# Kernel optimization log

Measured on AMD Instinct MI355X. Metric: run time of the kernel, lower is better.

## Reference

```python
import jax, jax.numpy as jnp
import numpy as np

HID = 64        # HIDDEN_DIM
SLOTS = 6       # MEMORY_SLOTS
V = 64          # VOCAB_SIZE
NH = 2          # attention heads
THRESH = 0.5    # STAGE1_THRESH
EPS = 1e-5      # LayerNorm eps (torch default)


def setup_inputs() -> dict:
    key = jax.random.key(0)
    ks = jax.random.split(key, 16)
    B, L = 64, 1024
    def n(k, shape, s=0.05):
        return jax.random.normal(k, shape, jnp.float32) * s
    return {
        'seq':    jax.random.randint(ks[0], (B, L), 0, V),
        'query':  jax.random.randint(ks[1], (B,), 0, V),
        'target': jax.random.randint(ks[2], (B,), 0, V),
        # TinyEncoder params
        'embed':   n(ks[3], (V, HID)),
        'wqkv':    n(ks[4], (3 * HID, HID)), 'bqkv': jnp.zeros(3 * HID, jnp.float32),
        'wo_attn': n(ks[5], (HID, HID)),     'bo_attn': jnp.zeros(HID, jnp.float32),
        'w_ff1':   n(ks[6], (2 * HID, HID)), 'b_ff1': jnp.zeros(2 * HID, jnp.float32),
        'w_ff2':   n(ks[7], (HID, 2 * HID)), 'b_ff2': jnp.zeros(HID, jnp.float32),
        'g1': jnp.ones(HID, jnp.float32), 'be1': jnp.zeros(HID, jnp.float32),
        'g2': jnp.ones(HID, jnp.float32), 'be2': jnp.zeros(HID, jnp.float32),
        # gates
        'w_s1': n(ks[8], (1, HID)), 'b_s1': jnp.zeros(1, jnp.float32),
        'w_s2': n(ks[9], (1, HID)), 'b_s2': jnp.zeros(1, jnp.float32),
        # MemoryReader
        'w_qr': n(ks[10], (HID, HID)), 'b_qr': jnp.zeros(HID, jnp.float32),
        'w_or': n(ks[11], (V, HID)),   'b_or': jnp.zeros(V, jnp.float32),
        # query embedding
        'q_embed': n(ks[12], (V, HID)),
    }


def _layernorm(x, g, b):
    m = x.mean(-1, keepdims=True)
    v = ((x - m) ** 2).mean(-1, keepdims=True)
    return (x - m) * jax.lax.rsqrt(v + EPS) * g + b


def _mha(h, wqkv, bqkv, wo, bo):
    B, L, H = h.shape
    d = H // NH
    qkv = h @ wqkv.T + bqkv                      # [B,L,3H]
    q, k, v = jnp.split(qkv, 3, axis=-1)
    q = q.reshape(B, L, NH, d)
    k = k.reshape(B, L, NH, d)
    v = v.reshape(B, L, NH, d)
    scores = jnp.einsum('bqhd,bkhd->bhqk', q, k) / jnp.sqrt(jnp.float32(d))
    w = jax.nn.softmax(scores, axis=-1)          # [B,NH,L,L]
    o = jnp.einsum('bhqk,bkhd->bqhd', w, v).reshape(B, L, H)
    return o @ wo.T + bo


def reference(seq, query, target, embed, wqkv, bqkv, wo_attn, bo_attn,
              w_ff1, b_ff1, w_ff2, b_ff2, g1, be1, g2, be2,
              w_s1, b_s1, w_s2, b_s2, w_qr, b_qr, w_or, b_or, q_embed):
    # --- TinyEncoder ---
    h = embed[seq]                                           # [B,L,H]
    a = _mha(h, wqkv, bqkv, wo_attn, bo_attn)
    h = _layernorm(h + a, g1, be1)
    ff = jax.nn.relu(h @ w_ff1.T + b_ff1) @ w_ff2.T + b_ff2
    hidden = _layernorm(h + ff, g2, be2)                     # [B,L,H]

    # --- two-stage selection (vectorized; dead s1-branch elided) ---
    s1 = jax.nn.sigmoid(jnp.squeeze(hidden @ w_s1.T + b_s1, -1))   # [B,L]
    keep = (s1 > THRESH).astype(hidden.dtype)
    s2 = jax.nn.sigmoid(jnp.squeeze(hidden @ w_s2.T + b_s2, -1))
    s2f = s2 * keep
    _, topk = jax.lax.top_k(s2f, SLOTS)                            # [B,SLOTS]

    # --- gather memory slots ---
    mem = jnp.take_along_axis(hidden, topk[:, :, None], axis=1)    # [B,SLOTS,H]

    # --- MemoryReader ---
    q_h = q_embed[query]                                           # [B,H]
    q = q_h @ w_qr.T + b_qr                                        # [B,H]
    scores = (q[:, None, :] * mem).sum(-1) / jnp.sqrt(jnp.float32(HID))  # [B,SLOTS]
    w = jax.nn.softmax(scores, axis=-1)
    ctx = (w[:, :, None] * mem).sum(1)                             # [B,H]
    logits = ctx @ w_or.T + b_or                                   # [B,V]

    # --- cross entropy (mean) ---
    logp = jax.nn.log_softmax(logits, axis=-1)
    loss = -jnp.take_along_axis(logp, target[:, None], axis=1).mean()
    return loss
```

## Files before the change

kernel.cpp:

```cpp
#include <hip/hip_runtime.h>

#define DEV __device__ __forceinline__

DEV float wsum(float v){
  #pragma unroll
  for (int o = 32; o; o >>= 1) v += __shfl_xor(v, o, 64);
  return v;
}
DEV float wmax(float v){
  #pragma unroll
  for (int o = 32; o; o >>= 1) v = fmaxf(v, __shfl_xor(v, o, 64));
  return v;
}

__global__ __launch_bounds__(256) void k_prep(
    const int* __restrict__ seq, const float* __restrict__ embed,
    const float* __restrict__ wqkv, const float* __restrict__ bqkv,
    float* __restrict__ qkv_tab, float* __restrict__ cnt_f){
  const int b = blockIdx.x, tid = threadIdx.x;
  __shared__ float emb[64];
  __shared__ int hh[64];
  if (tid < 64){ emb[tid] = embed[b*64 + tid]; hh[tid] = 0; }
  __syncthreads();
  for (int i = tid; i < 1024; i += 256) atomicAdd(&hh[seq[b*1024 + i]], 1);
  if (tid < 192){
    const float4* w4 = (const float4*)(wqkv + tid*64);
    float acc = bqkv[tid];
    #pragma unroll
    for (int k = 0; k < 16; ++k){
      float4 w = w4[k];
      acc += w.x*emb[4*k] + w.y*emb[4*k+1] + w.z*emb[4*k+2] + w.w*emb[4*k+3];
    }
    qkv_tab[b*192 + tid] = acc;
  }
  __syncthreads();
  if (tid < 64) cnt_f[b*64 + tid] = (float)hh[tid];
}

__global__ __launch_bounds__(256) void k_enc(
    const float* __restrict__ qkv_tab, const float* __restrict__ cnt_f,
    const float* __restrict__ embed,
    const float* __restrict__ wo_attn, const float* __restrict__ bo_attn,
    const float* __restrict__ w_ff1, const float* __restrict__ b_ff1,
    const float* __restrict__ w_ff2, const float* __restrict__ b_ff2,
    const float* __restrict__ g1, const float* __restrict__ be1,
    const float* __restrict__ g2, const float* __restrict__ be2,
    const float* __restrict__ w_s1, const float* __restrict__ b_s1,
    const float* __restrict__ w_s2, const float* __restrict__ b_s2,
    float* __restrict__ hidden_tab, float* __restrict__ s2f_tab){
  const int b = blockIdx.x >> 2, quarter = blockIdx.x & 3;
  const int tid = threadIdx.x, wave = tid >> 6, lane = tid & 63;

  __shared__ float k_lds[64*65];
  __shared__ float v_lds[64*65];
  __shared__ float wo_lds[64*65];
  __shared__ float ff1_lds[128*65];
  __shared__ float ff2_lds[64*129];
  __shared__ float cnt_lds[64];
  __shared__ float xbuf[4][64];
  __shared__ float ybuf[4][128];

  for (int i = tid; i < 4096; i += 256){
    int r = i >> 6, c = i & 63;
    k_lds[r*65 + c]  = qkv_tab[r*192 + 64 + c];
    v_lds[r*65 + c]  = qkv_tab[r*192 + 128 + c];
    wo_lds[r*65 + c] = wo_attn[i];
  }
  for (int i = tid; i < 8192; i += 256){
    ff1_lds[(i >> 6)*65 + (i & 63)]   = w_ff1[i];
    ff2_lds[(i >> 7)*129 + (i & 127)] = w_ff2[i];
  }
  if (tid < 64) cnt_lds[tid] = cnt_f[b*64 + tid];
  __syncthreads();

  const float g1v = g1[lane],  be1v = be1[lane];
  const float g2v = g2[lane],  be2v = be2[lane];
  const float bov = bo_attn[lane], bf2v = b_ff2[lane];
  const float bf1a = b_ff1[lane], bf1b = b_ff1[64 + lane];
  const float ws1v = w_s1[lane], ws2v = w_s2[lane];
  const float bs1 = b_s1[0], bs2 = b_s2[0];
  const float cme = cnt_lds[lane];
  const bool  pres = cme > 0.f;
  const float sc = 0.17677669529663687f;

  #pragma unroll 1
  for (int it = 0; it < 4; ++it){
    const int tok = quarter*16 + wave*4 + it;
    const float qreg = qkv_tab[tok*192 + lane];
    float s0 = 0.f, s1v = 0.f;
    #pragma unroll
    for (int d = 0; d < 32; ++d){
      float q0 = __shfl(qreg, d, 64);
      float q1 = __shfl(qreg, 32 + d, 64);
      s0  += q0 * k_lds[lane*65 + d];
      s1v += q1 * k_lds[lane*65 + 32 + d];
    }
    s0 *= sc; s1v *= sc;
    float m0 = wmax(pres ? s0  : -1e30f);
    float m1 = wmax(pres ? s1v : -1e30f);
    float p0 = pres ? cme * __expf(s0  - m0) : 0.f;
    float p1 = pres ? cme * __expf(s1v - m1) : 0.f;
    float d0 = wsum(p0), d1 = wsum(p1);
    float o = 0.f;
    #pragma unroll
    for (int t = 0; t < 64; ++t){
      float a0 = __shfl(p0, t, 64);
      float a1 = __shfl(p1, t, 64);
      o += (lane < 32 ? a0 : a1) * v_lds[t*65 + lane];
    }
    o /= (lane < 32 ? d0 : d1);
    float a = bov;
    #pragma unroll
    for (int k = 0; k < 64; ++k) a += wo_lds[lane*65 + k] * __shfl(o, k, 64);
    float x = embed[tok*64 + lane] + a;
    float mu = wsum(x) * 0.015625f;
    float xm = x - mu;
    float var = wsum(xm*xm) * 0.015625f;
    float xn = xm * rsqrtf(var + 1e-5f) * g1v + be1v;
    xbuf[wave][lane] = xn;
    __builtin_amdgcn_wave_barrier();
    float y0 = bf1a, y1 = bf1b;
    #pragma unroll
    for (int k = 0; k < 64; ++k){
      float xk = xbuf[wave][k];
      y0 += ff1_lds[lane*65 + k] * xk;
      y1 += ff1_lds[(lane + 64)*65 + k] * xk;
    }
    y0 = fmaxf(y0, 0.f); y1 = fmaxf(y1, 0.f);
    ybuf[wave][lane] = y0; ybuf[wave][64 + lane] = y1;
    __builtin_amdgcn_wave_barrier();
    float z = bf2v;
    #pragma unroll
    for (int j = 0; j < 128; ++j) z += ff2_lds[lane*129 + j] * ybuf[wave][j];
    float r = xn + z;
    float mu2 = wsum(r) * 0.015625f;
    float rm = r - mu2;
    float var2 = wsum(rm*rm) * 0.015625f;
    float hid = rm * rsqrtf(var2 + 1e-5f) * g2v + be2v;
    float t1 = wsum(hid * ws1v) + bs1;
    float t2 = wsum(hid * ws2v) + bs2;
    float sg1 = 1.f / (1.f + __expf(-t1));
    float sg2 = 1.f / (1.f + __expf(-t2));
    float s2f = (sg1 > 0.5f) ? sg2 : 0.f;

    hidden_tab[(b*64 + tok)*64 + lane] = hid;
    if (lane == 0) s2f_tab[b*64 + tok] = s2f;
  }
}

__global__ __launch_bounds__(64) void k_sel(
    const int* __restrict__ seq, const int* __restrict__ query,
    const int* __restrict__ target,
    const float* __restrict__ hidden_tab, const float* __restrict__ s2f_tab,
    const float* __restrict__ w_qr, const float* __restrict__ b_qr,
    const float* __restrict__ w_or, const float* __restrict__ b_or,
    const float* __restrict__ q_embed, float* __restrict__ partial){
  const int b = blockIdx.x, lane = threadIdx.x;
  __shared__ float s2_lds[64];
  s2_lds[lane] = s2f_tab[b*64 + lane];
  __builtin_amdgcn_wave_barrier();

  float vals[16];
  #pragma unroll
  for (int j = 0; j < 16; ++j){
    int tk = seq[b*1024 + j*64 + lane];
    vals[j] = s2_lds[tk];
  }
  int sel[6];
  #pragma unroll
  for (int r = 0; r < 6; ++r){
    float bv = -1.f; int bi = 1 << 30;
    #pragma unroll
    for (int j = 0; j < 16; ++j){
      float v = vals[j]; int i = (j << 6) | lane;
      if (v > bv || (v == bv && i < bi)){ bv = v; bi = i; }
    }
    #pragma unroll
    for (int o = 32; o; o >>= 1){
      float ov = __shfl_xor(bv, o, 64);
      int   oi = __shfl_xor(bi, o, 64);
      if (ov > bv || (ov == bv && oi < bi)){ bv = ov; bi = oi; }
    }
    sel[r] = bi;
    int jw = bi >> 6, lw = bi & 63;
    if (lane == lw){
      #pragma unroll
      for (int j = 0; j < 16; ++j) if (j == jw) vals[j] = -1.f;
    }
  }

  float mem[6];
  #pragma unroll
  for (int s = 0; s < 6; ++s){
    int tk = seq[b*1024 + sel[s]];
    mem[s] = hidden_tab[(b*64 + tk)*64 + lane];
  }
  float qe = q_embed[query[b]*64 + lane];
  float qv = b_qr[lane];
  #pragma unroll
  for (int k = 0; k < 64; ++k) qv += w_qr[lane*64 + k] * __shfl(qe, k, 64);
  float scv[6];
  #pragma unroll
  for (int s = 0; s < 6; ++s) scv[s] = wsum(qv * mem[s]) * 0.125f;
  float mx = scv[0];
  #pragma unroll
  for (int s = 1; s < 6; ++s) mx = fmaxf(mx, scv[s]);
  float e[6], se = 0.f;
  #pragma unroll
  for (int s = 0; s < 6; ++s){ e[s] = __expf(scv[s] - mx); se += e[s]; }
  float ctx = 0.f;
  #pragma unroll
  for (int s = 0; s < 6; ++s) ctx += (e[s] / se) * mem[s];
  float lg = b_or[lane];
  #pragma unroll
  for (int k = 0; k < 64; ++k) lg += w_or[lane*64 + k] * __shfl(ctx, k, 64);
  float lm = wmax(lg);
  float ss = wsum(__expf(lg - lm));
  float lt = __shfl(lg, target[b], 64);
  if (lane == 0) partial[b] = -(lt - lm - __logf(ss));
}

__global__ __launch_bounds__(64) void k_final(const float* __restrict__ partial,
                                              float* __restrict__ out){
  float v = partial[threadIdx.x];
  v = wsum(v);
  if (threadIdx.x == 0) out[0] = v * 0.015625f;
}

extern "C" void kernel_launch(void* const* d_in, const int* in_sizes, int n_in,
                              void* d_out, int out_size, void* d_ws, size_t ws_size,
                              hipStream_t stream){
  const int*   seq     = (const int*)  d_in[0];
  const int*   query   = (const int*)  d_in[1];
  const int*   target  = (const int*)  d_in[2];
  const float* embed   = (const float*)d_in[3];
  const float* wqkv    = (const float*)d_in[4];
  const float* bqkv    = (const float*)d_in[5];
  const float* wo_attn = (const float*)d_in[6];
  const float* bo_attn = (const float*)d_in[7];
  const float* w_ff1   = (const float*)d_in[8];
  const float* b_ff1   = (const float*)d_in[9];
  const float* w_ff2   = (const float*)d_in[10];
  const float* b_ff2   = (const float*)d_in[11];
  const float* g1      = (const float*)d_in[12];
  const float* be1     = (const float*)d_in[13];
  const float* g2      = (const float*)d_in[14];
  const float* be2     = (const float*)d_in[15];
  const float* w_s1    = (const float*)d_in[16];
  const float* b_s1    = (const float*)d_in[17];
  const float* w_s2    = (const float*)d_in[18];
  const float* b_s2    = (const float*)d_in[19];
  const float* w_qr    = (const float*)d_in[20];
  const float* b_qr    = (const float*)d_in[21];
  const float* w_or    = (const float*)d_in[22];
  const float* b_or    = (const float*)d_in[23];
  const float* q_embed = (const float*)d_in[24];

  float* ws = (float*)d_ws;
  float* qkv_tab    = ws;
  float* cnt_f      = ws + 12288;
  float* hidden_tab = ws + 16384;
  float* s2f_tab    = ws + 278528;
  float* partial    = ws + 282624;

  k_prep<<<64, 256, 0, stream>>>(seq, embed, wqkv, bqkv, qkv_tab, cnt_f);
  k_enc<<<256, 256, 0, stream>>>(qkv_tab, cnt_f, embed, wo_attn, bo_attn,
                                 w_ff1, b_ff1, w_ff2, b_ff2, g1, be1, g2, be2,
                                 w_s1, b_s1, w_s2, b_s2, hidden_tab, s2f_tab);
  k_sel<<<64, 64, 0, stream>>>(seq, query, target, hidden_tab, s2f_tab,
                               w_qr, b_qr, w_or, b_or, q_embed, partial);
  k_final<<<1, 64, 0, stream>>>(partial, (float*)d_out);
}
```

Baseline: 150.1 us.

## Use one wave per token, drop final kernel via atomic loss, stage weights in LDS

The encoder kernel now launches 1024 threads per block with one wave per token, replacing the four-token sequential loop per wave. Query and probability broadcasts go through LDS instead of lane shuffles, and the dot products use multiple accumulators to expose more ILP. The reduction kernel is removed: the output is zeroed in the prep kernel and each selection block adds its scaled loss atomically. The selection kernel also stages w_qr and w_or into padded LDS. The trade-off is that the larger blocks reload the weights into LDS for every 16 tokens, and the atomic sum makes the result order nondeterministic.

```diff
diff --git a/kernel.cpp b/kernel.cpp
--- a/kernel.cpp
+++ b/kernel.cpp
@@ -13,31 +13,36 @@
   return v;
 }
 
-__global__ __launch_bounds__(256) void k_prep(
+__global__ __launch_bounds__(1024) void k_prep(
     const int* __restrict__ seq, const float* __restrict__ embed,
     const float* __restrict__ wqkv, const float* __restrict__ bqkv,
-    float* __restrict__ qkv_tab, float* __restrict__ cnt_f){
+    float* __restrict__ qkv_tab, float* __restrict__ cnt_f,
+    float* __restrict__ out){
   const int b = blockIdx.x, tid = threadIdx.x;
+  if (b == 0 && tid == 0) out[0] = 0.f;
   __shared__ float emb[64];
   __shared__ int hh[64];
   if (tid < 64){ emb[tid] = embed[b*64 + tid]; hh[tid] = 0; }
   __syncthreads();
-  for (int i = tid; i < 1024; i += 256) atomicAdd(&hh[seq[b*1024 + i]], 1);
+  atomicAdd(&hh[seq[b*1024 + tid]], 1);
   if (tid < 192){
     const float4* w4 = (const float4*)(wqkv + tid*64);
-    float acc = bqkv[tid];
+    float a0 = bqkv[tid], a1 = 0.f, a2 = 0.f, a3 = 0.f;
     #pragma unroll
-    for (int k = 0; k < 16; ++k){
-      float4 w = w4[k];
-      acc += w.x*emb[4*k] + w.y*emb[4*k+1] + w.z*emb[4*k+2] + w.w*emb[4*k+3];
+    for (int k = 0; k < 16; k += 4){
+      float4 wa = w4[k],   wb = w4[k+1], wc = w4[k+2], wd = w4[k+3];
+      a0 += wa.x*emb[4*k]    + wa.y*emb[4*k+1]  + wa.z*emb[4*k+2]  + wa.w*emb[4*k+3];
+      a1 += wb.x*emb[4*k+4]  + wb.y*emb[4*k+5]  + wb.z*emb[4*k+6]  + wb.w*emb[4*k+7];
+      a2 += wc.x*emb[4*k+8]  + wc.y*emb[4*k+9]  + wc.z*emb[4*k+10] + wc.w*emb[4*k+11];
+      a3 += wd.x*emb[4*k+12] + wd.y*emb[4*k+13] + wd.z*emb[4*k+14] + wd.w*emb[4*k+15];
     }
-    qkv_tab[b*192 + tid] = acc;
+    qkv_tab[b*192 + tid] = (a0+a1)+(a2+a3);
   }
   __syncthreads();
   if (tid < 64) cnt_f[b*64 + tid] = (float)hh[tid];
 }
 
-__global__ __launch_bounds__(256) void k_enc(
+__global__ __launch_bounds__(1024, 4) void k_enc(
     const float* __restrict__ qkv_tab, const float* __restrict__ cnt_f,
     const float* __restrict__ embed,
     const float* __restrict__ wo_attn, const float* __restrict__ bo_attn,
@@ -57,16 +62,16 @@
   __shared__ float ff1_lds[128*65];
   __shared__ float ff2_lds[64*129];
   __shared__ float cnt_lds[64];
-  __shared__ float xbuf[4][64];
-  __shared__ float ybuf[4][128];
-
-  for (int i = tid; i < 4096; i += 256){
+  __shared__ float xbuf[16][64];
+  __shared__ float pbuf[16][128];
+
+  for (int i = tid; i < 4096; i += 1024){
     int r = i >> 6, c = i & 63;
     k_lds[r*65 + c]  = qkv_tab[r*192 + 64 + c];
     v_lds[r*65 + c]  = qkv_tab[r*192 + 128 + c];
     wo_lds[r*65 + c] = wo_attn[i];
   }
-  for (int i = tid; i < 8192; i += 256){
+  for (int i = tid; i < 8192; i += 1024){
     ff1_lds[(i >> 6)*65 + (i & 63)]   = w_ff1[i];
     ff2_lds[(i >> 7)*129 + (i & 127)] = w_ff2[i];
   }
@@ -82,70 +87,90 @@
   const float cme = cnt_lds[lane];
   const bool  pres = cme > 0.f;
   const float sc = 0.17677669529663687f;
-
-  #pragma unroll 1
-  for (int it = 0; it < 4; ++it){
-    const int tok = quarter*16 + wave*4 + it;
-    const float qreg = qkv_tab[tok*192 + lane];
-    float s0 = 0.f, s1v = 0.f;
-    #pragma unroll
-    for (int d = 0; d < 32; ++d){
-      float q0 = __shfl(qreg, d, 64);
-      float q1 = __shfl(qreg, 32 + d, 64);
-      s0  += q0 * k_lds[lane*65 + d];
-      s1v += q1 * k_lds[lane*65 + 32 + d];
-    }
-    s0 *= sc; s1v *= sc;
-    float m0 = wmax(pres ? s0  : -1e30f);
-    float m1 = wmax(pres ? s1v : -1e30f);
-    float p0 = pres ? cme * __expf(s0  - m0) : 0.f;
-    float p1 = pres ? cme * __expf(s1v - m1) : 0.f;
-    float d0 = wsum(p0), d1 = wsum(p1);
-    float o = 0.f;
-    #pragma unroll
-    for (int t = 0; t < 64; ++t){
-      float a0 = __shfl(p0, t, 64);
-      float a1 = __shfl(p1, t, 64);
-      o += (lane < 32 ? a0 : a1) * v_lds[t*65 + lane];
-    }
-    o /= (lane < 32 ? d0 : d1);
-    float a = bov;
-    #pragma unroll
-    for (int k = 0; k < 64; ++k) a += wo_lds[lane*65 + k] * __shfl(o, k, 64);
-    float x = embed[tok*64 + lane] + a;
-    float mu = wsum(x) * 0.015625f;
-    float xm = x - mu;
-    float var = wsum(xm*xm) * 0.015625f;
-    float xn = xm * rsqrtf(var + 1e-5f) * g1v + be1v;
-    xbuf[wave][lane] = xn;
-    __builtin_amdgcn_wave_barrier();
-    float y0 = bf1a, y1 = bf1b;
-    #pragma unroll
-    for (int k = 0; k < 64; ++k){
-      float xk = xbuf[wave][k];
-      y0 += ff1_lds[lane*65 + k] * xk;
-      y1 += ff1_lds[(lane + 64)*65 + k] * xk;
-    }
-    y0 = fmaxf(y0, 0.f); y1 = fmaxf(y1, 0.f);
-    ybuf[wave][lane] = y0; ybuf[wave][64 + lane] = y1;
-    __builtin_amdgcn_wave_barrier();
-    float z = bf2v;
-    #pragma unroll
-    for (int j = 0; j < 128; ++j) z += ff2_lds[lane*129 + j] * ybuf[wave][j];
-    float r = xn + z;
-    float mu2 = wsum(r) * 0.015625f;
-    float rm = r - mu2;
-    float var2 = wsum(rm*rm) * 0.015625f;
-    float hid = rm * rsqrtf(var2 + 1e-5f) * g2v + be2v;
-    float t1 = wsum(hid * ws1v) + bs1;
-    float t2 = wsum(hid * ws2v) + bs2;
-    float sg1 = 1.f / (1.f + __expf(-t1));
-    float sg2 = 1.f / (1.f + __expf(-t2));
-    float s2f = (sg1 > 0.5f) ? sg2 : 0.f;
-
-    hidden_tab[(b*64 + tok)*64 + lane] = hid;
-    if (lane == 0) s2f_tab[b*64 + tok] = s2f;
-  }
+  const int   tok = quarter*16 + wave;
+
+  const float qreg = qkv_tab[tok*192 + lane];
+  xbuf[wave][lane] = qreg;
+  __builtin_amdgcn_wave_barrier();
+  float s0a = 0.f, s0b = 0.f, s1a = 0.f, s1b = 0.f;
+  #pragma unroll
+  for (int d = 0; d < 32; d += 2){
+    s0a += xbuf[wave][d]      * k_lds[lane*65 + d];
+    s0b += xbuf[wave][d+1]    * k_lds[lane*65 + d + 1];
+    s1a += xbuf[wave][32+d]   * k_lds[lane*65 + 32 + d];
+    s1b += xbuf[wave][32+d+1] * k_lds[lane*65 + 32 + d + 1];
+  }
+  float s0  = (s0a + s0b) * sc;
+  float s1v = (s1a + s1b) * sc;
+  float m0 = wmax(pres ? s0  : -1e30f);
+  float m1 = wmax(pres ? s1v : -1e30f);
+  float p0 = pres ? cme * __expf(s0  - m0) : 0.f;
+  float p1 = pres ? cme * __expf(s1v - m1) : 0.f;
+  float d0 = wsum(p0), d1 = wsum(p1);
+  pbuf[wave][lane] = p0; pbuf[wave][64 + lane] = p1;
+  __builtin_amdgcn_wave_barrier();
+  const int pb = (lane & 32) << 1;
+  float o0 = 0.f, o1 = 0.f, o2 = 0.f, o3 = 0.f;
+  #pragma unroll
+  for (int t = 0; t < 64; t += 4){
+    o0 += pbuf[wave][pb + t]     * v_lds[t*65 + lane];
+    o1 += pbuf[wave][pb + t + 1] * v_lds[(t+1)*65 + lane];
+    o2 += pbuf[wave][pb + t + 2] * v_lds[(t+2)*65 + lane];
+    o3 += pbuf[wave][pb + t + 3] * v_lds[(t+3)*65 + lane];
+  }
+  float o = ((o0 + o1) + (o2 + o3)) / (lane < 32 ? d0 : d1);
+  xbuf[wave][lane] = o;
+  __builtin_amdgcn_wave_barrier();
+  float a0 = bov, a1 = 0.f, a2 = 0.f, a3 = 0.f;
+  #pragma unroll
+  for (int k = 0; k < 64; k += 4){
+    a0 += wo_lds[lane*65 + k]     * xbuf[wave][k];
+    a1 += wo_lds[lane*65 + k + 1] * xbuf[wave][k+1];
+    a2 += wo_lds[lane*65 + k + 2] * xbuf[wave][k+2];
+    a3 += wo_lds[lane*65 + k + 3] * xbuf[wave][k+3];
+  }
+  float a = (a0 + a1) + (a2 + a3);
+  float x = embed[tok*64 + lane] + a;
+  float mu = wsum(x) * 0.015625f;
+  float xm = x - mu;
+  float var = wsum(xm*xm) * 0.015625f;
+  float xn = xm * rsqrtf(var + 1e-5f) * g1v + be1v;
+  xbuf[wave][lane] = xn;
+  __builtin_amdgcn_wave_barrier();
+  float y0a = bf1a, y0b = 0.f, y1a = bf1b, y1b = 0.f;
+  #pragma unroll
+  for (int k = 0; k < 64; k += 2){
+    float xk0 = xbuf[wave][k], xk1 = xbuf[wave][k+1];
+    y0a += ff1_lds[lane*65 + k]          * xk0;
+    y0b += ff1_lds[lane*65 + k + 1]      * xk1;
+    y1a += ff1_lds[(lane+64)*65 + k]     * xk0;
+    y1b += ff1_lds[(lane+64)*65 + k + 1] * xk1;
+  }
+  float y0 = fmaxf(y0a + y0b, 0.f), y1 = fmaxf(y1a + y1b, 0.f);
+  pbuf[wave][lane] = y0; pbuf[wave][64 + lane] = y1;
+  __builtin_amdgcn_wave_barrier();
+  float z0 = bf2v, z1 = 0.f, z2 = 0.f, z3 = 0.f;
+  #pragma unroll
+  for (int j = 0; j < 128; j += 4){
+    z0 += ff2_lds[lane*129 + j]     * pbuf[wave][j];
+    z1 += ff2_lds[lane*129 + j + 1] * pbuf[wave][j+1];
+    z2 += ff2_lds[lane*129 + j + 2] * pbuf[wave][j+2];
+    z3 += ff2_lds[lane*129 + j + 3] * pbuf[wave][j+3];
+  }
+  float z = (z0 + z1) + (z2 + z3);
+  float r = xn + z;
+  float mu2 = wsum(r) * 0.015625f;
+  float rm = r - mu2;
+  float var2 = wsum(rm*rm) * 0.015625f;
+  float hid = rm * rsqrtf(var2 + 1e-5f) * g2v + be2v;
+  float t1 = wsum(hid * ws1v) + bs1;
+  float t2 = wsum(hid * ws2v) + bs2;
+  float sg1 = 1.f / (1.f + __expf(-t1));
+  float sg2 = 1.f / (1.f + __expf(-t2));
+  float s2f = (sg1 > 0.5f) ? sg2 : 0.f;
+
+  hidden_tab[(b*64 + tok)*64 + lane] = hid;
+  if (lane == 0) s2f_tab[b*64 + tok] = s2f;
 }
 
 __global__ __launch_bounds__(64) void k_sel(
@@ -154,10 +179,17 @@
     const float* __restrict__ hidden_tab, const float* __restrict__ s2f_tab,
     const float* __restrict__ w_qr, const float* __restrict__ b_qr,
     const float* __restrict__ w_or, const float* __restrict__ b_or,
-    const float* __restrict__ q_embed, float* __restrict__ partial){
+    const float* __restrict__ q_embed, float* __restrict__ out){
   const int b = blockIdx.x, lane = threadIdx.x;
   __shared__ float s2_lds[64];
+  __shared__ float wq_lds[64*65];
+  __shared__ float wor_lds[64*65];
   s2_lds[lane] = s2f_tab[b*64 + lane];
+  #pragma unroll 8
+  for (int j = 0; j < 64; ++j){
+    wq_lds[j*65 + lane]  = w_qr[j*64 + lane];
+    wor_lds[j*65 + lane] = w_or[j*64 + lane];
+  }
   __builtin_amdgcn_wave_barrier();
 
   float vals[16];
@@ -196,9 +228,15 @@
     mem[s] = hidden_tab[(b*64 + tk)*64 + lane];
   }
   float qe = q_embed[query[b]*64 + lane];
-  float qv = b_qr[lane];
-  #pragma unroll
-  for (int k = 0; k < 64; ++k) qv += w_qr[lane*64 + k] * __shfl(qe, k, 64);
+  float qv0 = b_qr[lane], qv1 = 0.f, qv2 = 0.f, qv3 = 0.f;
+  #pragma unroll
+  for (int k = 0; k < 64; k += 4){
+    qv0 += wq_lds[lane*65 + k]     * __shfl(qe, k, 64);
+    qv1 += wq_lds[lane*65 + k + 1] * __shfl(qe, k+1, 64);
+    qv2 += wq_lds[lane*65 + k + 2] * __shfl(qe, k+2, 64);
+    qv3 += wq_lds[lane*65 + k + 3] * __shfl(qe, k+3, 64);
+  }
+  float qv = (qv0 + qv1) + (qv2 + qv3);
   float scv[6];
   #pragma unroll
   for (int s = 0; s < 6; ++s) scv[s] = wsum(qv * mem[s]) * 0.125f;
@@ -211,20 +249,19 @@
   float ctx = 0.f;
   #pragma unroll
   for (int s = 0; s < 6; ++s) ctx += (e[s] / se) * mem[s];
-  float lg = b_or[lane];
-  #pragma unroll
-  for (int k = 0; k < 64; ++k) lg += w_or[lane*64 + k] * __shfl(ctx, k, 64);
+  float l0 = b_or[lane], l1 = 0.f, l2 = 0.f, l3 = 0.f;
+  #pragma unroll
+  for (int k = 0; k < 64; k += 4){
+    l0 += wor_lds[lane*65 + k]     * __shfl(ctx, k, 64);
+    l1 += wor_lds[lane*65 + k + 1] * __shfl(ctx, k+1, 64);
+    l2 += wor_lds[lane*65 + k + 2] * __shfl(ctx, k+2, 64);
+    l3 += wor_lds[lane*65 + k + 3] * __shfl(ctx, k+3, 64);
+  }
+  float lg = (l0 + l1) + (l2 + l3);
   float lm = wmax(lg);
   float ss = wsum(__expf(lg - lm));
   float lt = __shfl(lg, target[b], 64);
-  if (lane == 0) partial[b] = -(lt - lm - __logf(ss));
-}
-
-__global__ __launch_bounds__(64) void k_final(const float* __restrict__ partial,
-                                              float* __restrict__ out){
-  float v = partial[threadIdx.x];
-  v = wsum(v);
-  if (threadIdx.x == 0) out[0] = v * 0.015625f;
+  if (lane == 0) atomicAdd(out, -(lt - lm - __logf(ss)) * 0.015625f);
 }
 
 extern "C" void kernel_launch(void* const* d_in, const int* in_sizes, int n_in,
@@ -261,13 +298,13 @@
   float* cnt_f      = ws + 12288;
   float* hidden_tab = ws + 16384;
   float* s2f_tab    = ws + 278528;
-  float* partial    = ws + 282624;
-
-  k_prep<<<64, 256, 0, stream>>>(seq, embed, wqkv, bqkv, qkv_tab, cnt_f);
-  k_enc<<<256, 256, 0, stream>>>(qkv_tab, cnt_f, embed, wo_attn, bo_attn,
-                                 w_ff1, b_ff1, w_ff2, b_ff2, g1, be1, g2, be2,
-                                 w_s1, b_s1, w_s2, b_s2, hidden_tab, s2f_tab);
+
+  float* out = (float*)d_out;
+
+  k_prep<<<64, 1024, 0, stream>>>(seq, embed, wqkv, bqkv, qkv_tab, cnt_f, out);
+  k_enc<<<256, 1024, 0, stream>>>(qkv_tab, cnt_f, embed, wo_attn, bo_attn,
+                                  w_ff1, b_ff1, w_ff2, b_ff2, g1, be1, g2, be2,
+                                  w_s1, b_s1, w_s2, b_s2, hidden_tab, s2f_tab);
   k_sel<<<64, 64, 0, stream>>>(seq, query, target, hidden_tab, s2f_tab,
-                               w_qr, b_qr, w_or, b_or, q_embed, partial);
-  k_final<<<1, 64, 0, stream>>>(partial, (float*)d_out);
-}
+                               w_qr, b_qr, w_or, b_or, q_embed, out);
+}
```

After: 136.9 us. 8.8% less time.
